# Kernel optimization log

Measured on AMD Instinct MI355X. Metric: run time of the kernel, lower is better.

## Reference

```python
import jax, jax.numpy as jnp
import numpy as np

B = 262144   # batch of polygon pairs
N = 8        # vertices per polygon
TWO_PI = 2.0 * np.pi


def sort_poly(p):
    # sort vertices CCW by angle about the centroid (repo's sort_poly)
    c = jnp.mean(p, axis=-2, keepdims=True)
    v = p - c
    ang = jnp.arctan2(v[..., 1], v[..., 0])
    order = jnp.argsort(ang, axis=-1)
    return jnp.take_along_axis(p, order[..., None], axis=-2)


def shoelace(p):
    # signed area, positive for CCW polygons: [..., K, 2] -> [...]
    q = jnp.roll(p, -1, axis=-2)
    return 0.5 * jnp.sum(p[..., 0] * q[..., 1] - p[..., 1] * q[..., 0], axis=-1)


def points_inside(pts, poly):
    # pts [B,K,2], poly [B,N,2] convex CCW -> bool [B,K]
    a = poly[:, None, :, :]
    e = jnp.roll(poly, -1, axis=1)[:, None, :, :] - a
    w = pts[:, :, None, :] - a
    cr = e[..., 0] * w[..., 1] - e[..., 1] * w[..., 0]
    return jnp.all(cr >= -1e-6, axis=-1)


def edge_intersections(pa, pb):
    # all pairwise edge-edge intersection points: -> pts [B,N*N,2], ok [B,N*N]
    bsz, n, _ = pa.shape
    p1 = pa[:, :, None, :]
    d1 = jnp.roll(pa, -1, axis=1)[:, :, None, :] - p1
    q1 = pb[:, None, :, :]
    d2 = jnp.roll(pb, -1, axis=1)[:, None, :, :] - q1
    denom = d1[..., 0] * d2[..., 1] - d1[..., 1] * d2[..., 0]
    safe = jnp.where(jnp.abs(denom) < 1e-9, 1.0, denom)
    r = q1 - p1
    t = (r[..., 0] * d2[..., 1] - r[..., 1] * d2[..., 0]) / safe
    u = (r[..., 0] * d1[..., 1] - r[..., 1] * d1[..., 0]) / safe
    ok = (jnp.abs(denom) >= 1e-9) & (t >= 0.0) & (t <= 1.0) & (u >= 0.0) & (u <= 1.0)
    pts = p1 + t[..., None] * d1
    return pts.reshape(bsz, n * n, 2), ok.reshape(bsz, n * n)


def convex_intersection_area(pa, pb):
    # intersection of two convex CCW polygons: candidate vertices are
    # (a-verts inside b) + (b-verts inside a) + edge-edge intersections,
    # sorted by angle around their centroid, shoelace with masked padding.
    ia = points_inside(pa, pb)
    ib = points_inside(pb, pa)
    xpts, xok = edge_intersections(pa, pb)
    cand = jnp.concatenate([pa, pb, xpts], axis=1)          # [B, 2N+N^2, 2]
    mask = jnp.concatenate([ia, ib, xok], axis=1)
    cnt = jnp.sum(mask, axis=1)
    mf = mask[..., None].astype(cand.dtype)
    ctr = jnp.sum(cand * mf, axis=1) / jnp.maximum(cnt, 1).astype(cand.dtype)[..., None]
    v = cand - ctr[:, None, :]
    ang = jnp.where(mask, jnp.arctan2(v[..., 1], v[..., 0]), 1e9)  # invalid -> end
    order = jnp.argsort(ang, axis=1)
    cand = jnp.take_along_axis(cand, order[..., None], axis=1)
    mask = jnp.take_along_axis(mask, order, axis=1)
    cand = jnp.where(mask[..., None], cand, cand[:, 0:1, :])  # pad w/ first valid pt
    area = shoelace(cand)
    return jnp.where(cnt >= 3, jnp.maximum(area, 0.0), 0.0)


def hull_area_single(pts):
    # gift wrapping (Jarvis march) over M points, accumulating CCW shoelace sum
    m = pts.shape[0]
    start = jnp.lexsort((pts[:, 0], pts[:, 1]))[0]  # lowest y, tie-break lowest x

    def step(carry, _):
        cur, d, done, acc = carry
        cp = pts[cur]
        v = pts - cp
        dist2 = jnp.sum(v * v, axis=-1)
        ang = jnp.arctan2(d[0] * v[:, 1] - d[1] * v[:, 0],
                          d[0] * v[:, 0] + d[1] * v[:, 1])
        ang = jnp.where(dist2 < 1e-16, jnp.inf, jnp.mod(ang, TWO_PI))
        nxt = jnp.argmin(ang)
        npnt = pts[nxt]
        acc = acc + jnp.where(done, 0.0, cp[0] * npnt[1] - cp[1] * npnt[0])
        done = done | (nxt == start)
        return (nxt, npnt - cp, done, acc), None

    init = (start, jnp.array([1.0, 0.0], pts.dtype), jnp.array(False),
            jnp.zeros((), pts.dtype))
    (_, _, _, acc), _ = jax.lax.scan(step, init, None, length=m)
    return 0.5 * acc


def _make_convex(key, bsz, n):
    # random convex polygons: points on random ellipses at sorted angles
    k1, k2, k3, k4 = jax.random.split(key, 4)
    th = jnp.sort(jax.random.uniform(k1, (bsz, n)) * TWO_PI, axis=1)
    rx = 0.5 + 1.5 * jax.random.uniform(k2, (bsz, 1))
    ry = 0.5 + 1.5 * jax.random.uniform(k3, (bsz, 1))
    c = jax.random.uniform(k4, (bsz, 2)) * 2.0 - 1.0
    return c[:, None, :] + jnp.stack([rx * jnp.cos(th), ry * jnp.sin(th)], axis=-1)


def setup_inputs() -> dict:
    key = jax.random.key(0)
    ka, kb = jax.random.split(key)
    a = _make_convex(ka, B, N).astype(jnp.float32)
    b = _make_convex(kb, B, N).astype(jnp.float32)
    return {"a": a, "b": b}


def reference(a, b):
    pa = sort_poly(a)
    pb = sort_poly(b)
    area_a = shoelace(pa)
    area_b = shoelace(pb)
    inter = convex_intersection_area(pa, pb)     # [B]
    union = area_a + area_b - inter              # shapely a.union(b).area
    iou = inter / union
    all_pts = jnp.concatenate([a, b], axis=1)    # [B, 2N, 2]
    ch_area = jax.vmap(hull_area_single)(all_pts)
    ciou = iou - (ch_area - union) / ch_area
    return jnp.mean(ciou)                        # sum over batch / batch_size
```

## Files before the change

kernel.cpp:

```cpp
#include <hip/hip_runtime.h>

#define TPB 256

__global__ __launch_bounds__(TPB, 2) void ciou_main(
    const float* __restrict__ A,
    const float* __restrict__ Bq,
    double* __restrict__ partial,
    int nbatch, int tail)
{
    const int t = threadIdx.x;
    const int i0 = blockIdx.x * TPB + t;
    const bool live = !tail || (i0 < nbatch);
    const int i = live ? i0 : (nbatch - 1);

    float ax0,ax1,ax2,ax3,ax4,ax5,ax6,ax7;
    float ay0,ay1,ay2,ay3,ay4,ay5,ay6,ay7;
    float bx0,bx1,bx2,bx3,bx4,bx5,bx6,bx7;
    float by0,by1,by2,by3,by4,by5,by6,by7;
    {
        const float4* pa = (const float4*)(A + (size_t)i * 16);
        const float4* pb = (const float4*)(Bq + (size_t)i * 16);
        float4 q;
        q = pa[0]; ax0=q.x; ay0=q.y; ax1=q.z; ay1=q.w;
        q = pa[1]; ax2=q.x; ay2=q.y; ax3=q.z; ay3=q.w;
        q = pa[2]; ax4=q.x; ay4=q.y; ax5=q.z; ay5=q.w;
        q = pa[3]; ax6=q.x; ay6=q.y; ax7=q.z; ay7=q.w;
        q = pb[0]; bx0=q.x; by0=q.y; bx1=q.z; by1=q.w;
        q = pb[1]; bx2=q.x; by2=q.y; bx3=q.z; by3=q.w;
        q = pb[2]; bx4=q.x; by4=q.y; bx5=q.z; by5=q.w;
        q = pb[3]; bx6=q.x; by6=q.y; bx7=q.z; by7=q.w;
    }

#define MKEA(I,IN) float eax##I = ax##IN - ax##I, eay##I = ay##IN - ay##I;
#define MKEB(I,IN) float ebx##I = bx##IN - bx##I, eby##I = by##IN - by##I;
    MKEA(0,1) MKEA(1,2) MKEA(2,3) MKEA(3,4)
    MKEA(4,5) MKEA(5,6) MKEA(6,7) MKEA(7,0)
    MKEB(0,1) MKEB(1,2) MKEB(2,3) MKEB(3,4)
    MKEB(4,5) MKEB(5,6) MKEB(6,7) MKEB(7,0)
#define MKCA(I,IN) float ca##I = ax##I*ay##IN - ay##I*ax##IN;
#define MKCB(I,IN) float cb##I = bx##I*by##IN - by##I*bx##IN;
    MKCA(0,1) MKCA(1,2) MKCA(2,3) MKCA(3,4)
    MKCA(4,5) MKCA(5,6) MKCA(6,7) MKCA(7,0)
    MKCB(0,1) MKCB(1,2) MKCB(2,3) MKCB(3,4)
    MKCB(4,5) MKCB(5,6) MKCB(6,7) MKCB(7,0)
    float area_a = 0.5f * (((ca0+ca1)+(ca2+ca3)) + ((ca4+ca5)+(ca6+ca7)));
    float area_b = 0.5f * (((cb0+cb1)+(cb2+cb3)) + ((cb4+cb5)+(cb6+cb7)));

    float inter2 = 0.f;

#define HP(T0,T1,EX,EY,CC) { \
        float aa = EX*Py - EY*Px + (CC); \
        float bb = EX*Dy - EY*Dx; \
        float tc = __fdividef(-aa, bb); \
        float h = bb * 1e38f; \
        T0 = fmaxf(T0, fminf(tc, h)); \
        T1 = fminf(T1, fmaxf(tc, h)); }

#define HPB HP(t0a,t1a, ebx0,eby0,cb0) HP(t0b,t1b, ebx1,eby1,cb1) \
            HP(t0a,t1a, ebx2,eby2,cb2) HP(t0b,t1b, ebx3,eby3,cb3) \
            HP(t0a,t1a, ebx4,eby4,cb4) HP(t0b,t1b, ebx5,eby5,cb5) \
            HP(t0a,t1a, ebx6,eby6,cb6) HP(t0b,t1b, ebx7,eby7,cb7)
#define HPA HP(t0a,t1a, eax0,eay0,ca0) HP(t0b,t1b, eax1,eay1,ca1) \
            HP(t0a,t1a, eax2,eay2,ca2) HP(t0b,t1b, eax3,eay3,ca3) \
            HP(t0a,t1a, eax4,eay4,ca4) HP(t0b,t1b, eax5,eay5,ca5) \
            HP(t0a,t1a, eax6,eay6,ca6) HP(t0b,t1b, eax7,eay7,ca7)

#define EDGE(PX,PY,DX,DY,CPD,HPS) { \
        const float Px = (PX), Py = (PY); \
        const float Dx = (DX), Dy = (DY); \
        float t0a = 0.f, t1a = 1.f, t0b = 0.f, t1b = 1.f; \
        HPS \
        float dt = fminf(t1a, t1b) - fmaxf(t0a, t0b); \
        inter2 += fmaxf(dt, 0.f) * (CPD); }

    EDGE(ax0,ay0, eax0,eay0, ca0, HPB) EDGE(ax1,ay1, eax1,eay1, ca1, HPB)
    EDGE(ax2,ay2, eax2,eay2, ca2, HPB) EDGE(ax3,ay3, eax3,eay3, ca3, HPB)
    EDGE(ax4,ay4, eax4,eay4, ca4, HPB) EDGE(ax5,ay5, eax5,eay5, ca5, HPB)
    EDGE(ax6,ay6, eax6,eay6, ca6, HPB) EDGE(ax7,ay7, eax7,eay7, ca7, HPB)
    EDGE(bx0,by0, ebx0,eby0, cb0, HPA) EDGE(bx1,by1, ebx1,eby1, cb1, HPA)
    EDGE(bx2,by2, ebx2,eby2, cb2, HPA) EDGE(bx3,by3, ebx3,eby3, cb3, HPA)
    EDGE(bx4,by4, ebx4,eby4, cb4, HPA) EDGE(bx5,by5, ebx5,eby5, cb5, HPA)
    EDGE(bx6,by6, ebx6,eby6, cb6, HPA) EDGE(bx7,by7, ebx7,eby7, cb7, HPA)

    float inter = fmaxf(0.5f * inter2, 0.f);
    float uni = area_a + area_b - inter;
    float iou = __fdividef(inter, uni);

    float hbp = 0.f, hbm = 0.f, eSa = 0.f;
    float mbmin0=1e38f, mbmin1=1e38f, mbmin2=1e38f, mbmin3=1e38f,
          mbmin4=1e38f, mbmin5=1e38f, mbmin6=1e38f, mbmin7=1e38f;

#define BR2(EBXJ,EBYJ, EBXP,EBYP, BXJ,BYJ, MB) { \
        float Dx = (BXJ) - rax, Dy = (BYJ) - ray; \
        float c1 = Dx*reay - Dy*reax; \
        float c2 = Dx*peay - Dy*peax; \
        float c3 = Dx*(EBYJ) - Dy*(EBXJ); \
        float c4 = Dx*(EBYP) - Dy*(EBXP); \
        float cx = rax*(BYJ) - ray*(BXJ); \
        MB = fminf(MB, c3); \
        rmax = fmaxf(rmax, c1); \
        float mn = fminf(fminf(c1, -c2), fminf(c3, -c4)); \
        float mx = fmaxf(fmaxf(c1, -c2), fmaxf(c3, -c4)); \
        hbp += (mn >= 0.f) ? cx : 0.f; \
        hbm += (mx <= 0.f) ? cx : 0.f; }

#define BRROW(AXI,AYI, EAXI,EAYI, EAXP,EAYP, CAI) { \
        float rax = (AXI), ray = (AYI); \
        asm volatile("" : "+v"(rax), "+v"(ray) : "v"(hbp), "v"(hbm)); \
        const float reax = (EAXI), reay = (EAYI); \
        const float peax = (EAXP), peay = (EAYP); \
        float rmax = -1e38f; \
        BR2(ebx0,eby0, ebx7,eby7, bx0,by0, mbmin0) \
        BR2(ebx1,eby1, ebx0,eby0, bx1,by1, mbmin1) \
        BR2(ebx2,eby2, ebx1,eby1, bx2,by2, mbmin2) \
        BR2(ebx3,eby3, ebx2,eby2, bx3,by3, mbmin3) \
        BR2(ebx4,eby4, ebx3,eby3, bx4,by4, mbmin4) \
        BR2(ebx5,eby5, ebx4,eby4, bx5,by5, mbmin5) \
        BR2(ebx6,eby6, ebx5,eby5, bx6,by6, mbmin6) \
        BR2(ebx7,eby7, ebx6,eby6, bx7,by7, mbmin7) \
        eSa += (rmax <= 0.f) ? (CAI) : 0.f; }

    BRROW(ax0,ay0, eax0,eay0, eax7,eay7, ca0)
    BRROW(ax1,ay1, eax1,eay1, eax0,eay0, ca1)
    BRROW(ax2,ay2, eax2,eay2, eax1,eay1, ca2)
    BRROW(ax3,ay3, eax3,eay3, eax2,eay2, ca3)
    BRROW(ax4,ay4, eax4,eay4, eax3,eay3, ca4)
    BRROW(ax5,ay5, eax5,eay5, eax4,eay4, ca5)
    BRROW(ax6,ay6, eax6,eay6, eax5,eay5, ca6)
    BRROW(ax7,ay7, eax7,eay7, eax6,eay6, ca7)

    float eSb = (((mbmin0 >= 0.f ? cb0 : 0.f) + (mbmin1 >= 0.f ? cb1 : 0.f))
              +  ((mbmin2 >= 0.f ? cb2 : 0.f) + (mbmin3 >= 0.f ? cb3 : 0.f)))
              + (((mbmin4 >= 0.f ? cb4 : 0.f) + (mbmin5 >= 0.f ? cb5 : 0.f))
              +  ((mbmin6 >= 0.f ? cb6 : 0.f) + (mbmin7 >= 0.f ? cb7 : 0.f)));
    float ch = 0.5f * ((eSa + eSb) + (hbp - hbm));

    float val = iou - __fdividef(ch - uni, ch);
    float v = live ? val : 0.f;

    #pragma unroll
    for (int off = 32; off > 0; off >>= 1) v += __shfl_down(v, off);
    __shared__ float wsum[4];
    int lane = t & 63, wid = t >> 6;
    if (lane == 0) wsum[wid] = v;
    __syncthreads();
    if (t == 0) {
        partial[blockIdx.x] = (double)wsum[0] + (double)wsum[1]
                            + (double)wsum[2] + (double)wsum[3];
    }
}

__global__ __launch_bounds__(256) void ciou_finalize(
    const double* __restrict__ partial, float* __restrict__ out,
    int nparts, int nbatch)
{
    double v = 0.0;
    for (int j = threadIdx.x; j < nparts; j += 256) v += partial[j];
    #pragma unroll
    for (int off = 32; off > 0; off >>= 1) v += __shfl_down(v, off);
    __shared__ double s[4];
    int lane = threadIdx.x & 63, wid = threadIdx.x >> 6;
    if (lane == 0) s[wid] = v;
    __syncthreads();
    if (threadIdx.x == 0)
        out[0] = (float)((s[0] + s[1] + s[2] + s[3]) / (double)nbatch);
}

extern "C" void kernel_launch(void* const* d_in, const int* in_sizes, int n_in,
                              void* d_out, int out_size, void* d_ws, size_t ws_size,
                              hipStream_t stream) {
    const float* a = (const float*)d_in[0];
    const float* b = (const float*)d_in[1];
    float* out = (float*)d_out;
    int nbatch = in_sizes[0] / 16;
    int nblocks = (nbatch + TPB - 1) / TPB;
    int tail = (nblocks * TPB != nbatch) ? 1 : 0;
    double* partial = (double*)d_ws;
    ciou_main<<<nblocks, TPB, 0, stream>>>(a, b, partial, nbatch, tail);
    ciou_finalize<<<1, 256, 0, stream>>>(partial, out, nblocks, nbatch);
}
```

Baseline: 102.1 us.

## Split intersection and convex-hull work across two threads per polygon pair

Each block now handles 128 pairs with 256 threads. The first half of the block computes the clipped intersection area and IoU, and the second half computes the convex hull area, which it passes through shared memory. Edge vectors and cross terms are recomputed locally per role. The aim is shorter per-thread dependency chains, lower register pressure and more parallelism. In exchange, global loads are duplicated, a block barrier is added, and the two roles may be unevenly loaded.

```diff
diff --git a/kernel.cpp b/kernel.cpp
--- a/kernel.cpp
+++ b/kernel.cpp
@@ -1,6 +1,7 @@
 #include <hip/hip_runtime.h>
 
 #define TPB 256
+#define EPB 128
 
 __global__ __launch_bounds__(TPB, 2) void ciou_main(
     const float* __restrict__ A,
@@ -9,9 +10,11 @@
     int nbatch, int tail)
 {
     const int t = threadIdx.x;
-    const int i0 = blockIdx.x * TPB + t;
-    const bool live = !tail || (i0 < nbatch);
-    const int i = live ? i0 : (nbatch - 1);
+    const int el = t & 127;
+    const bool clipRole = t < 128;
+    const int e0 = blockIdx.x * EPB + el;
+    const bool live = !tail || (e0 < nbatch);
+    const int i = live ? e0 : (nbatch - 1);
 
     float ax0,ax1,ax2,ax3,ax4,ax5,ax6,ax7;
     float ay0,ay1,ay2,ay3,ay4,ay5,ay6,ay7;
@@ -31,22 +34,15 @@
         q = pb[3]; bx6=q.x; by6=q.y; bx7=q.z; by7=q.w;
     }
 
+    __shared__ float chbuf[EPB];
+    __shared__ float wsum[4];
+
+    float iou = 0.f, uni = 1.f;
+
+#define MKCA(I,IN) float ca##I = ax##I*ay##IN - ay##I*ax##IN;
+#define MKCB(I,IN) float cb##I = bx##I*by##IN - by##I*bx##IN;
 #define MKEA(I,IN) float eax##I = ax##IN - ax##I, eay##I = ay##IN - ay##I;
 #define MKEB(I,IN) float ebx##I = bx##IN - bx##I, eby##I = by##IN - by##I;
-    MKEA(0,1) MKEA(1,2) MKEA(2,3) MKEA(3,4)
-    MKEA(4,5) MKEA(5,6) MKEA(6,7) MKEA(7,0)
-    MKEB(0,1) MKEB(1,2) MKEB(2,3) MKEB(3,4)
-    MKEB(4,5) MKEB(5,6) MKEB(6,7) MKEB(7,0)
-#define MKCA(I,IN) float ca##I = ax##I*ay##IN - ay##I*ax##IN;
-#define MKCB(I,IN) float cb##I = bx##I*by##IN - by##I*bx##IN;
-    MKCA(0,1) MKCA(1,2) MKCA(2,3) MKCA(3,4)
-    MKCA(4,5) MKCA(5,6) MKCA(6,7) MKCA(7,0)
-    MKCB(0,1) MKCB(1,2) MKCB(2,3) MKCB(3,4)
-    MKCB(4,5) MKCB(5,6) MKCB(6,7) MKCB(7,0)
-    float area_a = 0.5f * (((ca0+ca1)+(ca2+ca3)) + ((ca4+ca5)+(ca6+ca7)));
-    float area_b = 0.5f * (((cb0+cb1)+(cb2+cb3)) + ((cb4+cb5)+(cb6+cb7)));
-
-    float inter2 = 0.f;
 
 #define HP(T0,T1,EX,EY,CC) { \
         float aa = EX*Py - EY*Px + (CC); \
@@ -65,30 +61,47 @@
             HP(t0a,t1a, eax4,eay4,ca4) HP(t0b,t1b, eax5,eay5,ca5) \
             HP(t0a,t1a, eax6,eay6,ca6) HP(t0b,t1b, eax7,eay7,ca7)
 
-#define EDGE(PX,PY,DX,DY,CPD,HPS) { \
+#define EDGE(PX,PY,QX,QY,CPD,HPS) { \
         const float Px = (PX), Py = (PY); \
-        const float Dx = (DX), Dy = (DY); \
+        const float Dx = (QX) - Px, Dy = (QY) - Py; \
         float t0a = 0.f, t1a = 1.f, t0b = 0.f, t1b = 1.f; \
         HPS \
         float dt = fminf(t1a, t1b) - fmaxf(t0a, t0b); \
         inter2 += fmaxf(dt, 0.f) * (CPD); }
 
-    EDGE(ax0,ay0, eax0,eay0, ca0, HPB) EDGE(ax1,ay1, eax1,eay1, ca1, HPB)
-    EDGE(ax2,ay2, eax2,eay2, ca2, HPB) EDGE(ax3,ay3, eax3,eay3, ca3, HPB)
-    EDGE(ax4,ay4, eax4,eay4, ca4, HPB) EDGE(ax5,ay5, eax5,eay5, ca5, HPB)
-    EDGE(ax6,ay6, eax6,eay6, ca6, HPB) EDGE(ax7,ay7, eax7,eay7, ca7, HPB)
-    EDGE(bx0,by0, ebx0,eby0, cb0, HPA) EDGE(bx1,by1, ebx1,eby1, cb1, HPA)
-    EDGE(bx2,by2, ebx2,eby2, cb2, HPA) EDGE(bx3,by3, ebx3,eby3, cb3, HPA)
-    EDGE(bx4,by4, ebx4,eby4, cb4, HPA) EDGE(bx5,by5, ebx5,eby5, cb5, HPA)
-    EDGE(bx6,by6, ebx6,eby6, cb6, HPA) EDGE(bx7,by7, ebx7,eby7, cb7, HPA)
-
-    float inter = fmaxf(0.5f * inter2, 0.f);
-    float uni = area_a + area_b - inter;
-    float iou = __fdividef(inter, uni);
-
-    float hbp = 0.f, hbm = 0.f, eSa = 0.f;
-    float mbmin0=1e38f, mbmin1=1e38f, mbmin2=1e38f, mbmin3=1e38f,
-          mbmin4=1e38f, mbmin5=1e38f, mbmin6=1e38f, mbmin7=1e38f;
+    if (clipRole) {
+        MKCA(0,1) MKCA(1,2) MKCA(2,3) MKCA(3,4)
+        MKCA(4,5) MKCA(5,6) MKCA(6,7) MKCA(7,0)
+        MKCB(0,1) MKCB(1,2) MKCB(2,3) MKCB(3,4)
+        MKCB(4,5) MKCB(5,6) MKCB(6,7) MKCB(7,0)
+        float area_a = 0.5f * (((ca0+ca1)+(ca2+ca3)) + ((ca4+ca5)+(ca6+ca7)));
+        float area_b = 0.5f * (((cb0+cb1)+(cb2+cb3)) + ((cb4+cb5)+(cb6+cb7)));
+        float inter2 = 0.f;
+        {
+            MKEB(0,1) MKEB(1,2) MKEB(2,3) MKEB(3,4)
+            MKEB(4,5) MKEB(5,6) MKEB(6,7) MKEB(7,0)
+            EDGE(ax0,ay0, ax1,ay1, ca0, HPB) EDGE(ax1,ay1, ax2,ay2, ca1, HPB)
+            EDGE(ax2,ay2, ax3,ay3, ca2, HPB) EDGE(ax3,ay3, ax4,ay4, ca3, HPB)
+            EDGE(ax4,ay4, ax5,ay5, ca4, HPB) EDGE(ax5,ay5, ax6,ay6, ca5, HPB)
+            EDGE(ax6,ay6, ax7,ay7, ca6, HPB) EDGE(ax7,ay7, ax0,ay0, ca7, HPB)
+        }
+        {
+            MKEA(0,1) MKEA(1,2) MKEA(2,3) MKEA(3,4)
+            MKEA(4,5) MKEA(5,6) MKEA(6,7) MKEA(7,0)
+            EDGE(bx0,by0, bx1,by1, cb0, HPA) EDGE(bx1,by1, bx2,by2, cb1, HPA)
+            EDGE(bx2,by2, bx3,by3, cb2, HPA) EDGE(bx3,by3, bx4,by4, cb3, HPA)
+            EDGE(bx4,by4, bx5,by5, cb4, HPA) EDGE(bx5,by5, bx6,by6, cb5, HPA)
+            EDGE(bx6,by6, bx7,by7, cb6, HPA) EDGE(bx7,by7, bx0,by0, cb7, HPA)
+        }
+        float inter = fmaxf(0.5f * inter2, 0.f);
+        uni = area_a + area_b - inter;
+        iou = __fdividef(inter, uni);
+    } else {
+        MKEB(0,1) MKEB(1,2) MKEB(2,3) MKEB(3,4)
+        MKEB(4,5) MKEB(5,6) MKEB(6,7) MKEB(7,0)
+        float hbp = 0.f, hbm = 0.f, eSa = 0.f;
+        float mbmin0=1e38f, mbmin1=1e38f, mbmin2=1e38f, mbmin3=1e38f,
+              mbmin4=1e38f, mbmin5=1e38f, mbmin6=1e38f, mbmin7=1e38f;
 
 #define BR2(EBXJ,EBYJ, EBXP,EBYP, BXJ,BYJ, MB) { \
         float Dx = (BXJ) - rax, Dy = (BYJ) - ray; \
@@ -104,11 +117,11 @@
         hbp += (mn >= 0.f) ? cx : 0.f; \
         hbm += (mx <= 0.f) ? cx : 0.f; }
 
-#define BRROW(AXI,AYI, EAXI,EAYI, EAXP,EAYP, CAI) { \
+#define BRROW(AXI,AYI, AXN,AYN, AXP,AYP) { \
         float rax = (AXI), ray = (AYI); \
         asm volatile("" : "+v"(rax), "+v"(ray) : "v"(hbp), "v"(hbm)); \
-        const float reax = (EAXI), reay = (EAYI); \
-        const float peax = (EAXP), peay = (EAYP); \
+        const float reax = (AXN) - (AXI), reay = (AYN) - (AYI); \
+        const float peax = (AXI) - (AXP), peay = (AYI) - (AYP); \
         float rmax = -1e38f; \
         BR2(ebx0,eby0, ebx7,eby7, bx0,by0, mbmin0) \
         BR2(ebx1,eby1, ebx0,eby0, bx1,by1, mbmin1) \
@@ -118,29 +131,38 @@
         BR2(ebx5,eby5, ebx4,eby4, bx5,by5, mbmin5) \
         BR2(ebx6,eby6, ebx5,eby5, bx6,by6, mbmin6) \
         BR2(ebx7,eby7, ebx6,eby6, bx7,by7, mbmin7) \
-        eSa += (rmax <= 0.f) ? (CAI) : 0.f; }
-
-    BRROW(ax0,ay0, eax0,eay0, eax7,eay7, ca0)
-    BRROW(ax1,ay1, eax1,eay1, eax0,eay0, ca1)
-    BRROW(ax2,ay2, eax2,eay2, eax1,eay1, ca2)
-    BRROW(ax3,ay3, eax3,eay3, eax2,eay2, ca3)
-    BRROW(ax4,ay4, eax4,eay4, eax3,eay3, ca4)
-    BRROW(ax5,ay5, eax5,eay5, eax4,eay4, ca5)
-    BRROW(ax6,ay6, eax6,eay6, eax5,eay5, ca6)
-    BRROW(ax7,ay7, eax7,eay7, eax6,eay6, ca7)
-
-    float eSb = (((mbmin0 >= 0.f ? cb0 : 0.f) + (mbmin1 >= 0.f ? cb1 : 0.f))
-              +  ((mbmin2 >= 0.f ? cb2 : 0.f) + (mbmin3 >= 0.f ? cb3 : 0.f)))
-              + (((mbmin4 >= 0.f ? cb4 : 0.f) + (mbmin5 >= 0.f ? cb5 : 0.f))
-              +  ((mbmin6 >= 0.f ? cb6 : 0.f) + (mbmin7 >= 0.f ? cb7 : 0.f)));
-    float ch = 0.5f * ((eSa + eSb) + (hbp - hbm));
-
-    float val = iou - __fdividef(ch - uni, ch);
-    float v = live ? val : 0.f;
+        float cai = rax*(AYN) - ray*(AXN); \
+        eSa += (rmax <= 0.f) ? cai : 0.f; }
+
+        BRROW(ax0,ay0, ax1,ay1, ax7,ay7)
+        BRROW(ax1,ay1, ax2,ay2, ax0,ay0)
+        BRROW(ax2,ay2, ax3,ay3, ax1,ay1)
+        BRROW(ax3,ay3, ax4,ay4, ax2,ay2)
+        BRROW(ax4,ay4, ax5,ay5, ax3,ay3)
+        BRROW(ax5,ay5, ax6,ay6, ax4,ay4)
+        BRROW(ax6,ay6, ax7,ay7, ax5,ay5)
+        BRROW(ax7,ay7, ax0,ay0, ax6,ay6)
+
+        MKCB(0,1) MKCB(1,2) MKCB(2,3) MKCB(3,4)
+        MKCB(4,5) MKCB(5,6) MKCB(6,7) MKCB(7,0)
+        float eSb = (((mbmin0 >= 0.f ? cb0 : 0.f) + (mbmin1 >= 0.f ? cb1 : 0.f))
+                  +  ((mbmin2 >= 0.f ? cb2 : 0.f) + (mbmin3 >= 0.f ? cb3 : 0.f)))
+                  + (((mbmin4 >= 0.f ? cb4 : 0.f) + (mbmin5 >= 0.f ? cb5 : 0.f))
+                  +  ((mbmin6 >= 0.f ? cb6 : 0.f) + (mbmin7 >= 0.f ? cb7 : 0.f)));
+        chbuf[el] = 0.5f * ((eSa + eSb) + (hbp - hbm));
+    }
+
+    __syncthreads();
+
+    float v = 0.f;
+    if (clipRole) {
+        float ch = chbuf[el];
+        float val = iou - __fdividef(ch - uni, ch);
+        v = live ? val : 0.f;
+    }
 
     #pragma unroll
     for (int off = 32; off > 0; off >>= 1) v += __shfl_down(v, off);
-    __shared__ float wsum[4];
     int lane = t & 63, wid = t >> 6;
     if (lane == 0) wsum[wid] = v;
     __syncthreads();
@@ -173,8 +195,8 @@
     const float* b = (const float*)d_in[1];
     float* out = (float*)d_out;
     int nbatch = in_sizes[0] / 16;
-    int nblocks = (nbatch + TPB - 1) / TPB;
-    int tail = (nblocks * TPB != nbatch) ? 1 : 0;
+    int nblocks = (nbatch + EPB - 1) / EPB;
+    int tail = (nblocks * EPB != nbatch) ? 1 : 0;
     double* partial = (double*)d_ws;
     ciou_main<<<nblocks, TPB, 0, stream>>>(a, b, partial, nbatch, tail);
     ciou_finalize<<<1, 256, 0, stream>>>(partial, out, nblocks, nbatch);
```

Result: slower. 104.4 us (+2.3%).

## Fuse edge-clipping and hull passes into one shared pairwise loop with reciprocal

Applied to the files above, without the earlier changes.

Merges the two separate 8x8 edge-pair passes (half-plane clipping for intersection area, and the hull/containment pass) into a single loop over A-vertex rows and B-edges. Each pair shares the cross products: one denominator is computed, its reciprocal is taken once, and it serves both the A-edge-vs-B clip and the B-edge-vs-A clip (with negated sign), so the per-pair division count drops. Edge vectors and shoelace terms for A are recomputed inline, which shortens live ranges. In exchange, 16 per-B-edge clip accumulators stay live across rows, which raises register pressure, and using rcp in place of a divide may change rounding slightly.

```diff
diff --git a/kernel.cpp b/kernel.cpp
--- a/kernel.cpp
+++ b/kernel.cpp
@@ -31,108 +31,70 @@
         q = pb[3]; bx6=q.x; by6=q.y; bx7=q.z; by7=q.w;
     }
 
-#define MKEA(I,IN) float eax##I = ax##IN - ax##I, eay##I = ay##IN - ay##I;
 #define MKEB(I,IN) float ebx##I = bx##IN - bx##I, eby##I = by##IN - by##I;
-    MKEA(0,1) MKEA(1,2) MKEA(2,3) MKEA(3,4)
-    MKEA(4,5) MKEA(5,6) MKEA(6,7) MKEA(7,0)
     MKEB(0,1) MKEB(1,2) MKEB(2,3) MKEB(3,4)
     MKEB(4,5) MKEB(5,6) MKEB(6,7) MKEB(7,0)
-#define MKCA(I,IN) float ca##I = ax##I*ay##IN - ay##I*ax##IN;
-#define MKCB(I,IN) float cb##I = bx##I*by##IN - by##I*bx##IN;
-    MKCA(0,1) MKCA(1,2) MKCA(2,3) MKCA(3,4)
-    MKCA(4,5) MKCA(5,6) MKCA(6,7) MKCA(7,0)
-    MKCB(0,1) MKCB(1,2) MKCB(2,3) MKCB(3,4)
-    MKCB(4,5) MKCB(5,6) MKCB(6,7) MKCB(7,0)
-    float area_a = 0.5f * (((ca0+ca1)+(ca2+ca3)) + ((ca4+ca5)+(ca6+ca7)));
-    float area_b = 0.5f * (((cb0+cb1)+(cb2+cb3)) + ((cb4+cb5)+(cb6+cb7)));
 
-    float inter2 = 0.f;
+    float t0b0=0.f,t0b1=0.f,t0b2=0.f,t0b3=0.f,t0b4=0.f,t0b5=0.f,t0b6=0.f,t0b7=0.f;
+    float t1b0=1.f,t1b1=1.f,t1b2=1.f,t1b3=1.f,t1b4=1.f,t1b5=1.f,t1b6=1.f,t1b7=1.f;
+    float mbmin0=1e38f,mbmin1=1e38f,mbmin2=1e38f,mbmin3=1e38f,
+          mbmin4=1e38f,mbmin5=1e38f,mbmin6=1e38f,mbmin7=1e38f;
+    float hbp = 0.f, hbm = 0.f, eSa = 0.f;
+    float inter2 = 0.f, areaA2 = 0.f;
 
-#define HP(T0,T1,EX,EY,CC) { \
-        float aa = EX*Py - EY*Px + (CC); \
-        float bb = EX*Dy - EY*Dx; \
-        float tc = __fdividef(-aa, bb); \
-        float h = bb * 1e38f; \
-        T0 = fmaxf(T0, fminf(tc, h)); \
-        T1 = fminf(T1, fmaxf(tc, h)); }
-
-#define HPB HP(t0a,t1a, ebx0,eby0,cb0) HP(t0b,t1b, ebx1,eby1,cb1) \
-            HP(t0a,t1a, ebx2,eby2,cb2) HP(t0b,t1b, ebx3,eby3,cb3) \
-            HP(t0a,t1a, ebx4,eby4,cb4) HP(t0b,t1b, ebx5,eby5,cb5) \
-            HP(t0a,t1a, ebx6,eby6,cb6) HP(t0b,t1b, ebx7,eby7,cb7)
-#define HPA HP(t0a,t1a, eax0,eay0,ca0) HP(t0b,t1b, eax1,eay1,ca1) \
-            HP(t0a,t1a, eax2,eay2,ca2) HP(t0b,t1b, eax3,eay3,ca3) \
-            HP(t0a,t1a, eax4,eay4,ca4) HP(t0b,t1b, eax5,eay5,ca5) \
-            HP(t0a,t1a, eax6,eay6,ca6) HP(t0b,t1b, eax7,eay7,ca7)
-
-#define EDGE(PX,PY,DX,DY,CPD,HPS) { \
-        const float Px = (PX), Py = (PY); \
-        const float Dx = (DX), Dy = (DY); \
-        float t0a = 0.f, t1a = 1.f, t0b = 0.f, t1b = 1.f; \
-        HPS \
-        float dt = fminf(t1a, t1b) - fmaxf(t0a, t0b); \
-        inter2 += fmaxf(dt, 0.f) * (CPD); }
-
-    EDGE(ax0,ay0, eax0,eay0, ca0, HPB) EDGE(ax1,ay1, eax1,eay1, ca1, HPB)
-    EDGE(ax2,ay2, eax2,eay2, ca2, HPB) EDGE(ax3,ay3, eax3,eay3, ca3, HPB)
-    EDGE(ax4,ay4, eax4,eay4, ca4, HPB) EDGE(ax5,ay5, eax5,eay5, ca5, HPB)
-    EDGE(ax6,ay6, eax6,eay6, ca6, HPB) EDGE(ax7,ay7, eax7,eay7, ca7, HPB)
-    EDGE(bx0,by0, ebx0,eby0, cb0, HPA) EDGE(bx1,by1, ebx1,eby1, cb1, HPA)
-    EDGE(bx2,by2, ebx2,eby2, cb2, HPA) EDGE(bx3,by3, ebx3,eby3, cb3, HPA)
-    EDGE(bx4,by4, ebx4,eby4, cb4, HPA) EDGE(bx5,by5, ebx5,eby5, cb5, HPA)
-    EDGE(bx6,by6, ebx6,eby6, cb6, HPA) EDGE(bx7,by7, ebx7,eby7, cb7, HPA)
-
-    float inter = fmaxf(0.5f * inter2, 0.f);
-    float uni = area_a + area_b - inter;
-    float iou = __fdividef(inter, uni);
-
-    float hbp = 0.f, hbm = 0.f, eSa = 0.f;
-    float mbmin0=1e38f, mbmin1=1e38f, mbmin2=1e38f, mbmin3=1e38f,
-          mbmin4=1e38f, mbmin5=1e38f, mbmin6=1e38f, mbmin7=1e38f;
-
-#define BR2(EBXJ,EBYJ, EBXP,EBYP, BXJ,BYJ, MB) { \
-        float Dx = (BXJ) - rax, Dy = (BYJ) - ray; \
+#define PAIR(J,JP) { \
+        float Dx = bx##J - rax, Dy = by##J - ray; \
+        float ee = ebx##J*reay - eby##J*reax; \
+        float rr = __builtin_amdgcn_rcpf(ee); \
         float c1 = Dx*reay - Dy*reax; \
+        float c3 = Dx*eby##J - Dy*ebx##J; \
         float c2 = Dx*peay - Dy*peax; \
-        float c3 = Dx*(EBYJ) - Dy*(EBXJ); \
-        float c4 = Dx*(EBYP) - Dy*(EBXP); \
-        float cx = rax*(BYJ) - ray*(BXJ); \
-        MB = fminf(MB, c3); \
+        float c4 = Dx*eby##JP - Dy*ebx##JP; \
+        float h = ee * 1e38f; \
+        float tc1 = -c3 * rr; \
+        t0a = fmaxf(t0a, fminf(tc1, h)); \
+        t1a = fminf(t1a, fmaxf(tc1, h)); \
+        float tc2 = -c1 * rr; \
+        t0b##J = fmaxf(t0b##J, fminf(tc2, -h)); \
+        t1b##J = fminf(t1b##J, fmaxf(tc2, -h)); \
+        mbmin##J = fminf(mbmin##J, c3); \
         rmax = fmaxf(rmax, c1); \
         float mn = fminf(fminf(c1, -c2), fminf(c3, -c4)); \
         float mx = fmaxf(fmaxf(c1, -c2), fmaxf(c3, -c4)); \
+        float cx = rax*by##J - ray*bx##J; \
         hbp += (mn >= 0.f) ? cx : 0.f; \
         hbm += (mx <= 0.f) ? cx : 0.f; }
 
-#define BRROW(AXI,AYI, EAXI,EAYI, EAXP,EAYP, CAI) { \
-        float rax = (AXI), ray = (AYI); \
+#define ROW(I,IN,IP) { \
+        float rax = ax##I, ray = ay##I; \
         asm volatile("" : "+v"(rax), "+v"(ray) : "v"(hbp), "v"(hbm)); \
-        const float reax = (EAXI), reay = (EAYI); \
-        const float peax = (EAXP), peay = (EAYP); \
-        float rmax = -1e38f; \
-        BR2(ebx0,eby0, ebx7,eby7, bx0,by0, mbmin0) \
-        BR2(ebx1,eby1, ebx0,eby0, bx1,by1, mbmin1) \
-        BR2(ebx2,eby2, ebx1,eby1, bx2,by2, mbmin2) \
-        BR2(ebx3,eby3, ebx2,eby2, bx3,by3, mbmin3) \
-        BR2(ebx4,eby4, ebx3,eby3, bx4,by4, mbmin4) \
-        BR2(ebx5,eby5, ebx4,eby4, bx5,by5, mbmin5) \
-        BR2(ebx6,eby6, ebx5,eby5, bx6,by6, mbmin6) \
-        BR2(ebx7,eby7, ebx6,eby6, bx7,by7, mbmin7) \
-        eSa += (rmax <= 0.f) ? (CAI) : 0.f; }
+        const float reax = ax##IN - rax, reay = ay##IN - ray; \
+        const float peax = rax - ax##IP, peay = ray - ay##IP; \
+        float t0a = 0.f, t1a = 1.f, rmax = -1e38f; \
+        PAIR(0,7) PAIR(1,0) PAIR(2,1) PAIR(3,2) \
+        PAIR(4,3) PAIR(5,4) PAIR(6,5) PAIR(7,6) \
+        float cai = rax*ay##IN - ray*ax##IN; \
+        areaA2 += cai; \
+        float dt = t1a - t0a; \
+        inter2 += fmaxf(dt, 0.f) * cai; \
+        eSa += (rmax <= 0.f) ? cai : 0.f; }
 
-    BRROW(ax0,ay0, eax0,eay0, eax7,eay7, ca0)
-    BRROW(ax1,ay1, eax1,eay1, eax0,eay0, ca1)
-    BRROW(ax2,ay2, eax2,eay2, eax1,eay1, ca2)
-    BRROW(ax3,ay3, eax3,eay3, eax2,eay2, ca3)
-    BRROW(ax4,ay4, eax4,eay4, eax3,eay3, ca4)
-    BRROW(ax5,ay5, eax5,eay5, eax4,eay4, ca5)
-    BRROW(ax6,ay6, eax6,eay6, eax5,eay5, ca6)
-    BRROW(ax7,ay7, eax7,eay7, eax6,eay6, ca7)
+    ROW(0,1,7) ROW(1,2,0) ROW(2,3,1) ROW(3,4,2)
+    ROW(4,5,3) ROW(5,6,4) ROW(6,7,5) ROW(7,0,6)
 
-    float eSb = (((mbmin0 >= 0.f ? cb0 : 0.f) + (mbmin1 >= 0.f ? cb1 : 0.f))
-              +  ((mbmin2 >= 0.f ? cb2 : 0.f) + (mbmin3 >= 0.f ? cb3 : 0.f)))
-              + (((mbmin4 >= 0.f ? cb4 : 0.f) + (mbmin5 >= 0.f ? cb5 : 0.f))
-              +  ((mbmin6 >= 0.f ? cb6 : 0.f) + (mbmin7 >= 0.f ? cb7 : 0.f)));
+    float areaB2 = 0.f, eSb = 0.f;
+#define BTAIL(J,JN) { \
+        float cbj = bx##J*by##JN - by##J*bx##JN; \
+        areaB2 += cbj; \
+        float dt = t1b##J - t0b##J; \
+        inter2 += fmaxf(dt, 0.f) * cbj; \
+        eSb += (mbmin##J >= 0.f) ? cbj : 0.f; }
+    BTAIL(0,1) BTAIL(1,2) BTAIL(2,3) BTAIL(3,4)
+    BTAIL(4,5) BTAIL(5,6) BTAIL(6,7) BTAIL(7,0)
+
+    float inter = fmaxf(0.5f * inter2, 0.f);
+    float uni = 0.5f * areaA2 + 0.5f * areaB2 - inter;
+    float iou = __fdividef(inter, uni);
     float ch = 0.5f * ((eSa + eSb) + (hbp - hbm));
 
     float val = iou - __fdividef(ch - uni, ch);
```

Result: faster. 90.41 us (-11.4%).
